# Optimization experiments

Hardware: AMD Instinct MI355X
Metric: run time of the kernel (lower is better)

## Reference

```python
import jax, jax.numpy as jnp
import numpy as np

N_HEADS = 4
NEG_SLOPE = 0.2  # DGL GATConv default leaky_relu slope


def setup_inputs() -> dict:
    key = jax.random.key(0)
    ks = jax.random.split(key, 12)
    N, E = 50000, 800000
    in_dim, time_dim, out_dim = 128, 128, 128
    d_head = out_dim // N_HEADS
    in_total = in_dim + time_dim
    h = jax.random.normal(ks[0], (N, in_dim), jnp.float32)
    time_tensor = jax.random.uniform(ks[1], (E,), jnp.float32)
    src = jax.random.randint(ks[2], (E,), 0, N, jnp.int32)
    dst = jax.random.randint(ks[3], (E,), 0, N, jnp.int32)
    # TimeEncoding: Linear(1, time_dim) with xavier weight, zero bias
    w_t = jax.random.normal(ks[4], (time_dim, 1), jnp.float32) * (6.0 / (1 + time_dim)) ** 0.5
    b_t = jnp.zeros((time_dim,), jnp.float32)
    # GATConv params
    W_fc = jax.random.normal(ks[5], (N_HEADS * d_head, in_total), jnp.float32) * (2.0 / in_total) ** 0.5
    attn_l = jax.random.normal(ks[6], (N_HEADS, d_head), jnp.float32) * 0.1
    attn_r = jax.random.normal(ks[7], (N_HEADS, d_head), jnp.float32) * 0.1
    W_res = jax.random.normal(ks[8], (N_HEADS * d_head, in_total), jnp.float32) * (2.0 / in_total) ** 0.5
    bias = jnp.zeros((N_HEADS * d_head,), jnp.float32)
    return {"h": h, "time_tensor": time_tensor, "src": src, "dst": dst,
            "num_nodes": N, "w_t": w_t, "b_t": b_t, "W_fc": W_fc,
            "attn_l": attn_l, "attn_r": attn_r, "W_res": W_res, "bias": bias}


def reference(h, time_tensor, src, dst, num_nodes, w_t, b_t, W_fc, attn_l, attn_r, W_res, bias):
    N = num_nodes
    E = src.shape[0]
    # Time encoding: cos(W t + b), per edge -> [E, time_dim]
    time_emb = jnp.cos(time_tensor[:, None] * w_t[:, 0][None, :] + b_t[None, :])
    # Mailbox mean of concat([src h, time_emb]) per dst node.
    # mean(concat) == concat(mean, mean), so sum the two halves separately.
    ones = jnp.ones((E,), h.dtype)
    deg = jax.ops.segment_sum(ones, dst, num_segments=N)  # [N]
    sum_h = jax.ops.segment_sum(h[src], dst, num_segments=N)       # [N, in_dim]
    sum_t = jax.ops.segment_sum(time_emb, dst, num_segments=N)     # [N, time_dim]
    inv_deg = 1.0 / jnp.maximum(deg, 1.0)
    h_time = jnp.concatenate([sum_h, sum_t], axis=1) * inv_deg[:, None]  # [N, in+time]
    # GATConv (eval mode, no dropout)
    d_head = W_fc.shape[0] // N_HEADS
    feat = (h_time @ W_fc.T).reshape(N, N_HEADS, d_head)  # [N,H,D]
    el = jnp.sum(feat * attn_l[None], axis=-1)  # [N,H]
    er = jnp.sum(feat * attn_r[None], axis=-1)  # [N,H]
    e = el[src] + er[dst]                        # [E,H]
    e = jnp.where(e > 0, e, NEG_SLOPE * e)
    # edge softmax over incoming edges of each dst node
    m = jax.ops.segment_max(e, dst, num_segments=N)  # [N,H]
    m = jnp.where(jnp.isfinite(m), m, 0.0)
    ex = jnp.exp(e - m[dst])
    denom = jax.ops.segment_sum(ex, dst, num_segments=N)
    a = ex / jnp.maximum(denom[dst], 1e-9)           # [E,H]
    rst = jax.ops.segment_sum(a[:, :, None] * feat[src], dst, num_segments=N)  # [N,H,D]
    res = (h_time @ W_res.T).reshape(N, N_HEADS, d_head)
    out = rst + res + bias.reshape(1, N_HEADS, d_head)
    out = jax.nn.elu(out)
    return out.reshape(N, -1)  # [N, out_dim]
```

## Files before the change

kernel.cpp:

```cpp
#include <hip/hip_runtime.h>
#include <math.h>

#define NH 4
#define NEG_SLOPE 0.2f
#define BKT_SHIFT 8
#define EPB 4096
#define CBLK 8192
#define INV2PI 0.15915494309189535f
#define LOG2E  1.4426950408889634f

typedef __attribute__((ext_vector_type(8))) short bf16x8;
typedef __attribute__((ext_vector_type(4))) float f32x4;

__device__ __forceinline__ float blo(unsigned u) { return __uint_as_float(u << 16); }
__device__ __forceinline__ float bhi(unsigned u) { return __uint_as_float(u & 0xFFFF0000u); }
__device__ __forceinline__ unsigned short rne(float f) {
    unsigned u = __float_as_uint(f);
    u += 0x7FFFu + ((u >> 16) & 1u);
    return (unsigned short)(u >> 16);
}
__device__ __forceinline__ unsigned pack2(float a, float b) {
    return (unsigned)rne(a) | ((unsigned)rne(b) << 16);
}

__global__ __launch_bounds__(256) void k_prep(
    const float* __restrict__ h, unsigned* __restrict__ hbu, int n_pairs,
    const float* __restrict__ Wfc, const float* __restrict__ Wres,
    unsigned* __restrict__ wcat,
    const float* __restrict__ w_t, const float* __restrict__ b_t,
    float2* __restrict__ w_s, float2* __restrict__ b_s,
    const int* __restrict__ dst, int* __restrict__ bkt_cnt, int E, int NB, int EB) {
    __shared__ int cnt[256];
    int tid = threadIdx.x;
    int t = blockIdx.x * blockDim.x + tid;
    if (t < n_pairs) {
        float2 v = ((const float2*)h)[t];
        hbu[t] = pack2(v.x, v.y);
    }
    if (t < 32768) {
        int col = t >> 7, kk = t & 127;
        const float* srcp = (col < 128) ? (Wfc + (size_t)col * 256)
                                        : (Wres + (size_t)(col - 128) * 256);
        float2 v = ((const float2*)srcp)[kk];
        wcat[t] = pack2(v.x, v.y);
    }
    if (t < 64) {
        float2 wv = ((const float2*)w_t)[t];
        float2 bv = ((const float2*)b_t)[t];
        w_s[t] = make_float2(wv.x * INV2PI, wv.y * INV2PI);
        b_s[t] = make_float2(bv.x * INV2PI, bv.y * INV2PI);
    }
    if (blockIdx.x < (unsigned)EB) {
        cnt[tid] = 0;
        __syncthreads();
        int q0 = (blockIdx.x * CBLK) >> 2;
#pragma unroll
        for (int k = 0; k < CBLK / 1024; k++) {
            int qi = q0 + k * 256 + tid;
            int base = qi * 4;
            if (base + 3 < E) {
                int4 d = ((const int4*)dst)[qi];
                atomicAdd(&cnt[d.x >> BKT_SHIFT], 1);
                atomicAdd(&cnt[d.y >> BKT_SHIFT], 1);
                atomicAdd(&cnt[d.z >> BKT_SHIFT], 1);
                atomicAdd(&cnt[d.w >> BKT_SHIFT], 1);
            } else {
                for (int e = base; e < E; e++) atomicAdd(&cnt[dst[e] >> BKT_SHIFT], 1);
            }
        }
        __syncthreads();
        if (tid < NB) {
            int c = cnt[tid];
            if (c) atomicAdd(bkt_cnt + tid, c);
        }
    }
}

__global__ __launch_bounds__(256) void k_bktscan(
    const int* __restrict__ bkt_cnt, int* __restrict__ bkt_start,
    int* __restrict__ bkt_cursor, int* __restrict__ row_start,
    int NB, int E, int N) {
    __shared__ int wsum[4];
    int tid = threadIdx.x, lane = tid & 63, wid = tid >> 6;
    int v = (tid < NB) ? bkt_cnt[tid] : 0;
    int x = v;
#pragma unroll
    for (int off = 1; off < 64; off <<= 1) {
        int y = __shfl_up(x, off, 64);
        if (lane >= off) x += y;
    }
    if (lane == 63) wsum[wid] = x;
    __syncthreads();
    if (tid == 0) {
        int s = 0;
#pragma unroll
        for (int k = 0; k < 4; k++) { int tk = wsum[k]; wsum[k] = s; s += tk; }
    }
    __syncthreads();
    int excl = wsum[wid] + x - v;
    if (tid < NB) { bkt_start[tid] = excl; bkt_cursor[tid] = excl; }
    if (tid == 0) { bkt_start[NB] = E; row_start[N] = E; }
}

__global__ __launch_bounds__(256) void k_binscatter(
    const int* __restrict__ src, const int* __restrict__ dst,
    const float* __restrict__ tt, int* __restrict__ bkt_cursor,
    uint2* __restrict__ staged, int E, int NB) {
    __shared__ int cnt[1024];
    __shared__ int basep[1024];
    int e0 = blockIdx.x * EPB;
    int tid = threadIdx.x;
    for (int b = tid; b < NB; b += 256) cnt[b] = 0;
    __syncthreads();
#pragma unroll
    for (int k = 0; k < EPB / 256; k++) {
        int e = e0 + k * 256 + tid;
        if (e < E) atomicAdd(&cnt[dst[e] >> BKT_SHIFT], 1);
    }
    __syncthreads();
    for (int b = tid; b < NB; b += 256) {
        int c = cnt[b];
        basep[b] = (c > 0) ? atomicAdd(bkt_cursor + b, c) : 0;
        cnt[b] = 0;
    }
    __syncthreads();
#pragma unroll
    for (int k = 0; k < EPB / 256; k++) {
        int e = e0 + k * 256 + tid;
        if (e < E) {
            int d = dst[e];
            int b = d >> BKT_SHIFT;
            int r = atomicAdd(&cnt[b], 1);
            unsigned tq = min((unsigned)(tt[e] * 32768.0f), 32767u);
            staged[basep[b] + r] =
                make_uint2(((unsigned)src[e] << 15) | tq, (unsigned)(d & 255));
        }
    }
}

__global__ __launch_bounds__(256) void k_binsort(
    const uint2* __restrict__ staged, const int* __restrict__ bkt_start,
    int* __restrict__ row_start, unsigned* __restrict__ est, int N) {
    __shared__ int cnt[256];
    __shared__ int cur[256];
    __shared__ int wsum[4];
    int b = blockIdx.x;
    int n0 = b << BKT_SHIFT;
    int tid = threadIdx.x;
    cnt[tid] = 0;
    __syncthreads();
    int s0 = bkt_start[b], s1 = bkt_start[b + 1];
    for (int p = s0 + tid; p < s1; p += 256)
        atomicAdd(&cnt[staged[p].y], 1);
    __syncthreads();
    int lane = tid & 63, wid = tid >> 6;
    int v = cnt[tid];
    int x = v;
#pragma unroll
    for (int off = 1; off < 64; off <<= 1) {
        int y = __shfl_up(x, off, 64);
        if (lane >= off) x += y;
    }
    if (lane == 63) wsum[wid] = x;
    __syncthreads();
    if (tid == 0) {
        int s = 0;
#pragma unroll
        for (int k = 0; k < 4; k++) { int tk = wsum[k]; wsum[k] = s; s += tk; }
    }
    __syncthreads();
    int excl = s0 + wsum[wid] + x - v;
    cur[tid] = excl;
    if (n0 + tid < N) row_start[n0 + tid] = excl;
    __syncthreads();
    for (int p = s0 + tid; p < s1; p += 256) {
        uint2 vv = staged[p];
        int pos = atomicAdd(&cur[vv.y], 1);
        est[pos] = vv.x;
    }
}

__device__ __forceinline__ void agg_edge(unsigned u, const uint4* __restrict__ h4,
                                         int i, float4 wa, float4 wb, float4 ba, float4 bb,
                                         float* aH, float* aT) {
    int s = (int)(u >> 15);
    float t = (float)((u & 0x7FFFu)) * (1.0f / 32768.0f) + (0.5f / 32768.0f);
    uint4 hv = h4[(size_t)s * 16 + i];
    aH[0] += blo(hv.x); aH[1] += bhi(hv.x);
    aH[2] += blo(hv.y); aH[3] += bhi(hv.y);
    aH[4] += blo(hv.z); aH[5] += bhi(hv.z);
    aH[6] += blo(hv.w); aH[7] += bhi(hv.w);
    aT[0] += __builtin_amdgcn_cosf(fmaf(t, wa.x, ba.x));
    aT[1] += __builtin_amdgcn_cosf(fmaf(t, wa.y, ba.y));
    aT[2] += __builtin_amdgcn_cosf(fmaf(t, wa.z, ba.z));
    aT[3] += __builtin_amdgcn_cosf(fmaf(t, wa.w, ba.w));
    aT[4] += __builtin_amdgcn_cosf(fmaf(t, wb.x, bb.x));
    aT[5] += __builtin_amdgcn_cosf(fmaf(t, wb.y, bb.y));
    aT[6] += __builtin_amdgcn_cosf(fmaf(t, wb.z, bb.z));
    aT[7] += __builtin_amdgcn_cosf(fmaf(t, wb.w, bb.w));
}

__device__ __forceinline__ void attn_edge(unsigned u, const uint4* __restrict__ f4,
                                          int i, int hd, const float* __restrict__ el,
                                          float erh, float* acc, float& den) {
    int s = (int)(u >> 15);
    float elh = el[(size_t)s * 4 + hd];
    uint4 fv = f4[(size_t)s * 16 + i];
    float w = elh + erh; w = w > 0.f ? w : NEG_SLOPE * w;
    float ex = __builtin_amdgcn_exp2f(w);
    acc[0] = fmaf(ex, blo(fv.x), acc[0]); acc[1] = fmaf(ex, bhi(fv.x), acc[1]);
    acc[2] = fmaf(ex, blo(fv.y), acc[2]); acc[3] = fmaf(ex, bhi(fv.y), acc[3]);
    acc[4] = fmaf(ex, blo(fv.z), acc[4]); acc[5] = fmaf(ex, bhi(fv.z), acc[5]);
    acc[6] = fmaf(ex, blo(fv.w), acc[6]); acc[7] = fmaf(ex, bhi(fv.w), acc[7]);
    den += ex;
}

__global__ __launch_bounds__(256) void k_agg(
    const unsigned* __restrict__ hbu, const unsigned* __restrict__ est,
    const int* __restrict__ row_start,
    const float2* __restrict__ w_s, const float2* __restrict__ b_s,
    unsigned* __restrict__ htu, int N) {
    int n = blockIdx.x * 4 + (threadIdx.x >> 6);
    if (n >= N) return;
    int lane = threadIdx.x & 63;
    int g = lane >> 4, i = lane & 15;
    int rs = row_start[n], re = row_start[n + 1];
    const uint4* h4 = (const uint4*)hbu;
    float4 wa = ((const float4*)w_s)[2 * i], wb = ((const float4*)w_s)[2 * i + 1];
    float4 ba = ((const float4*)b_s)[2 * i], bb = ((const float4*)b_s)[2 * i + 1];
    float aH[8] = {}, aT[8] = {};
    int nb = (re - rs) >> 4;
    int e = rs + g;
    for (int j = 0; j < nb; j++, e += 16) {
        unsigned u0 = est[e];
        unsigned u1 = est[e + 4];
        unsigned u2 = est[e + 8];
        unsigned u3 = est[e + 12];
        agg_edge(u0, h4, i, wa, wb, ba, bb, aH, aT);
        agg_edge(u1, h4, i, wa, wb, ba, bb, aH, aT);
        agg_edge(u2, h4, i, wa, wb, ba, bb, aH, aT);
        agg_edge(u3, h4, i, wa, wb, ba, bb, aH, aT);
    }
    for (; e < re; e += 4)
        agg_edge(est[e], h4, i, wa, wb, ba, bb, aH, aT);
#pragma unroll
    for (int off = 16; off <= 32; off <<= 1) {
#pragma unroll
        for (int k = 0; k < 8; k++) {
            aH[k] += __shfl_xor(aH[k], off, 64);
            aT[k] += __shfl_xor(aT[k], off, 64);
        }
    }
    if (g == 0) {
        int deg = re - rs;
        float idg = (deg > 0) ? 1.0f / (float)deg : 1.0f;
        uint4* ht4 = (uint4*)htu;
        uint4 oh, ot;
        oh.x = pack2(aH[0] * idg, aH[1] * idg);
        oh.y = pack2(aH[2] * idg, aH[3] * idg);
        oh.z = pack2(aH[4] * idg, aH[5] * idg);
        oh.w = pack2(aH[6] * idg, aH[7] * idg);
        ot.x = pack2(aT[0] * idg, aT[1] * idg);
        ot.y = pack2(aT[2] * idg, aT[3] * idg);
        ot.z = pack2(aT[4] * idg, aT[5] * idg);
        ot.w = pack2(aT[6] * idg, aT[7] * idg);
        ht4[(size_t)n * 32 + i]      = oh;
        ht4[(size_t)n * 32 + 16 + i] = ot;
    }
}

__global__ __launch_bounds__(256) void k_gemm(
    const unsigned short* __restrict__ ht, const unsigned short* __restrict__ wcat,
    unsigned short* __restrict__ feat, float* __restrict__ res_out,
    const float* __restrict__ attn_l, const float* __restrict__ attn_r,
    float* __restrict__ el, float* __restrict__ er, int N) {
    __shared__ __align__(16) unsigned short As[64 * 264];
    int tid = threadIdx.x;
    int row0 = blockIdx.x * 64;
    const uint4* src4 = (const uint4*)ht;
    for (int idx = tid; idx < 64 * 32; idx += 256) {
        int rl = idx >> 5, c16 = idx & 31;
        int gr = row0 + rl; if (gr >= N) gr = N - 1;
        uint4 v = src4[(size_t)gr * 32 + c16];
        *(uint4*)(As + rl * 264 + c16 * 8) = v;
    }
    __syncthreads();
    int wave = tid >> 6, lane = tid & 63;
    int r = lane & 15, q = lane >> 4;
    int colbase = wave * 64;
    const bf16x8* bbase = (const bf16x8*)wcat + (size_t)(colbase + r) * 32;
    const unsigned short* abase = As + r * 264 + q * 8;
    f32x4 acc[4][4] = {};
#pragma unroll
    for (int ks = 0; ks < 8; ks++) {
        bf16x8 a[4], b[4];
#pragma unroll
        for (int rt = 0; rt < 4; rt++)
            a[rt] = *(const bf16x8*)(abase + rt * (16 * 264) + ks * 32);
#pragma unroll
        for (int ct = 0; ct < 4; ct++)
            b[ct] = bbase[(size_t)ct * (16 * 32) + ks * 4 + q];
#pragma unroll
        for (int rt = 0; rt < 4; rt++)
#pragma unroll
            for (int ct = 0; ct < 4; ct++)
                acc[rt][ct] = __builtin_amdgcn_mfma_f32_16x16x32_bf16(a[rt], b[ct], acc[rt][ct], 0, 0, 0);
    }
    bool featw = (colbase < 128);
    float alv[4], arv[4];
    if (featw) {
#pragma unroll
        for (int ct = 0; ct < 4; ct++) {
            alv[ct] = attn_l[colbase + ct * 16 + r];
            arv[ct] = attn_r[colbase + ct * 16 + r];
        }
    }
#pragma unroll
    for (int rt = 0; rt < 4; rt++) {
#pragma unroll
        for (int reg = 0; reg < 4; reg++) {
            int row = row0 + rt * 16 + q * 4 + reg;
            float el0 = 0.f, el1 = 0.f, er0 = 0.f, er1 = 0.f;
#pragma unroll
            for (int ct = 0; ct < 4; ct++) {
                int col = colbase + ct * 16 + r;
                float v = acc[rt][ct][reg];
                if (featw) {
                    unsigned short pv = rne(v);
                    if (row < N) feat[(size_t)row * 128 + col] = pv;
                    float vr = blo((unsigned)pv);
                    if (ct < 2) { el0 = fmaf(vr, alv[ct], el0); er0 = fmaf(vr, arv[ct], er0); }
                    else        { el1 = fmaf(vr, alv[ct], el1); er1 = fmaf(vr, arv[ct], er1); }
                } else {
                    if (row < N) res_out[(size_t)row * 128 + (col - 128)] = v;
                }
            }
            if (featw) {
#pragma unroll
                for (int off = 1; off <= 8; off <<= 1) {
                    el0 += __shfl_xor(el0, off, 64);
                    el1 += __shfl_xor(el1, off, 64);
                    er0 += __shfl_xor(er0, off, 64);
                    er1 += __shfl_xor(er1, off, 64);
                }
                if (r == 0 && row < N) {
                    int hd0 = colbase >> 5;
                    el[(size_t)row * 4 + hd0]     = el0 * LOG2E;
                    el[(size_t)row * 4 + hd0 + 1] = el1 * LOG2E;
                    er[(size_t)row * 4 + hd0]     = er0 * LOG2E;
                    er[(size_t)row * 4 + hd0 + 1] = er1 * LOG2E;
                }
            }
        }
    }
}

__global__ __launch_bounds__(256) void k_attn(
    const unsigned* __restrict__ est, const int* __restrict__ row_start,
    const float* __restrict__ el, const float* __restrict__ er,
    const unsigned* __restrict__ featu, const float* __restrict__ bias,
    float* __restrict__ out, int N) {
    int n = blockIdx.x * 4 + (threadIdx.x >> 6);
    if (n >= N) return;
    int lane = threadIdx.x & 63;
    int g = lane >> 4, i = lane & 15;
    int hd = i >> 2;
    int rs = row_start[n], re = row_start[n + 1];
    float erh = er[(size_t)n * 4 + hd];
    const uint4* f4 = (const uint4*)featu;
    float acc[8] = {};
    float den = 0.f;
    int nb = (re - rs) >> 4;
    int e = rs + g;
    for (int j = 0; j < nb; j++, e += 16) {
        unsigned u0 = est[e];
        unsigned u1 = est[e + 4];
        unsigned u2 = est[e + 8];
        unsigned u3 = est[e + 12];
        attn_edge(u0, f4, i, hd, el, erh, acc, den);
        attn_edge(u1, f4, i, hd, el, erh, acc, den);
        attn_edge(u2, f4, i, hd, el, erh, acc, den);
        attn_edge(u3, f4, i, hd, el, erh, acc, den);
    }
    for (; e < re; e += 4)
        attn_edge(est[e], f4, i, hd, el, erh, acc, den);
#pragma unroll
    for (int off = 16; off <= 32; off <<= 1) {
#pragma unroll
        for (int k = 0; k < 8; k++) acc[k] += __shfl_xor(acc[k], off, 64);
        den += __shfl_xor(den, off, 64);
    }
    if (g == 0) {
        float id = 1.0f / fmaxf(den, 1e-9f);
        float* op = out + (size_t)n * 128 + i * 8;
        const float* bp = bias + i * 8;
        float4 o0 = ((const float4*)op)[0], o1 = ((const float4*)op)[1];
        float4 b0 = ((const float4*)bp)[0], b1 = ((const float4*)bp)[1];
        float4 r0, r1;
        r0.x = fmaf(acc[0], id, o0.x + b0.x);
        r0.y = fmaf(acc[1], id, o0.y + b0.y);
        r0.z = fmaf(acc[2], id, o0.z + b0.z);
        r0.w = fmaf(acc[3], id, o0.w + b0.w);
        r1.x = fmaf(acc[4], id, o1.x + b1.x);
        r1.y = fmaf(acc[5], id, o1.y + b1.y);
        r1.z = fmaf(acc[6], id, o1.z + b1.z);
        r1.w = fmaf(acc[7], id, o1.w + b1.w);
        r0.x = r0.x > 0.f ? r0.x : (__expf(r0.x) - 1.0f);
        r0.y = r0.y > 0.f ? r0.y : (__expf(r0.y) - 1.0f);
        r0.z = r0.z > 0.f ? r0.z : (__expf(r0.z) - 1.0f);
        r0.w = r0.w > 0.f ? r0.w : (__expf(r0.w) - 1.0f);
        r1.x = r1.x > 0.f ? r1.x : (__expf(r1.x) - 1.0f);
        r1.y = r1.y > 0.f ? r1.y : (__expf(r1.y) - 1.0f);
        r1.z = r1.z > 0.f ? r1.z : (__expf(r1.z) - 1.0f);
        r1.w = r1.w > 0.f ? r1.w : (__expf(r1.w) - 1.0f);
        ((float4*)op)[0] = r0;
        ((float4*)op)[1] = r1;
    }
}

extern "C" void kernel_launch(void* const* d_in, const int* in_sizes, int n_in,
                              void* d_out, int out_size, void* d_ws, size_t ws_size,
                              hipStream_t stream) {
    const float* h     = (const float*)d_in[0];
    const float* tt    = (const float*)d_in[1];
    const int*   src   = (const int*)d_in[2];
    const int*   dst   = (const int*)d_in[3];
    const float* w_t   = (const float*)d_in[5];
    const float* b_t   = (const float*)d_in[6];
    const float* W_fc  = (const float*)d_in[7];
    const float* al    = (const float*)d_in[8];
    const float* ar    = (const float*)d_in[9];
    const float* W_res = (const float*)d_in[10];
    const float* bias  = (const float*)d_in[11];

    int N = in_sizes[0] / 128;
    int E = in_sizes[1];
    int NB = (N + 255) >> BKT_SHIFT;
    int EB = (E + CBLK - 1) / CBLK;

    char* ws = (char*)d_ws;
    size_t off = 0;
    auto alloc = [&](size_t bytes) { void* p = ws + off; off = (off + bytes + 15) & ~(size_t)15; return p; };
    unsigned* htu     = (unsigned*)alloc((size_t)N * 128 * 4);
    unsigned* hbu     = (unsigned*)alloc((size_t)N * 64 * 4);
    unsigned* featu   = (unsigned*)alloc((size_t)N * 64 * 4);
    unsigned* wcat    = (unsigned*)alloc(32768 * 4);
    float2*   w_s     = (float2*)alloc(64 * 8);
    float2*   b_s     = (float2*)alloc(64 * 8);
    float*    el      = (float*)alloc((size_t)N * NH * 4);
    float*    er      = (float*)alloc((size_t)N * NH * 4);
    int*      row_st  = (int*)alloc((size_t)(N + 1) * 4);
    int*      bkt_cur = (int*)alloc((size_t)NB * 4);
    int*      bkt_cnt = (int*)alloc((size_t)NB * 4);
    int*      bkt_sta = (int*)alloc((size_t)(NB + 1) * 4);
    unsigned* est     = (unsigned*)alloc((size_t)E * 4);
    uint2*    staged  = (uint2*)featu;

    hipMemsetAsync(bkt_cnt, 0, (size_t)NB * 4, stream);

    int prep_n = N * 64;
    hipLaunchKernelGGL(k_prep, dim3((prep_n + 255) / 256), dim3(256), 0, stream,
                       h, hbu, prep_n, W_fc, W_res, wcat, w_t, b_t, w_s, b_s,
                       dst, bkt_cnt, E, NB, EB);
    hipLaunchKernelGGL(k_bktscan, dim3(1), dim3(256), 0, stream,
                       bkt_cnt, bkt_sta, bkt_cur, row_st, NB, E, N);
    hipLaunchKernelGGL(k_binscatter, dim3((E + EPB - 1) / EPB), dim3(256), 0, stream,
                       src, dst, tt, bkt_cur, staged, E, NB);
    hipLaunchKernelGGL(k_binsort, dim3(NB), dim3(256), 0, stream,
                       staged, bkt_sta, row_st, est, N);
    hipLaunchKernelGGL(k_agg, dim3((N + 3) / 4), dim3(256), 0, stream,
                       hbu, est, row_st, w_s, b_s, htu, N);
    hipLaunchKernelGGL(k_gemm, dim3((N + 63) / 64), dim3(256), 0, stream,
                       (const unsigned short*)htu, (const unsigned short*)wcat,
                       (unsigned short*)featu, (float*)d_out, al, ar, el, er, N);
    hipLaunchKernelGGL(k_attn, dim3((N + 3) / 4), dim3(256), 0, stream,
                       est, row_st, el, er, featu, bias, (float*)d_out, N);
}
```

Baseline: 252.1 us.

## Shrink GEMM tile to 16 rows without LDS and split el/er into separate kernel

The GEMM kernel drops its 64-row LDS-staged A tile and instead has each wave load its 16-row A fragment straight from global memory, launching four times as many blocks. The el/er attention-logit reduction moves out of the GEMM epilogue into a new small kernel that re-reads the bf16 feat rows. This removes the LDS stage, the shuffle reductions and register pressure from the GEMM, which may raise occupancy. In exchange it cuts reuse of each B-tile load across rows, repeats A loads across the four waves, and adds a kernel launch plus an extra pass over feat.

```diff
diff --git a/kernel.cpp b/kernel.cpp
--- a/kernel.cpp
+++ b/kernel.cpp
@@ -271,88 +271,62 @@
 
 __global__ __launch_bounds__(256) void k_gemm(
     const unsigned short* __restrict__ ht, const unsigned short* __restrict__ wcat,
-    unsigned short* __restrict__ feat, float* __restrict__ res_out,
-    const float* __restrict__ attn_l, const float* __restrict__ attn_r,
-    float* __restrict__ el, float* __restrict__ er, int N) {
-    __shared__ __align__(16) unsigned short As[64 * 264];
+    unsigned short* __restrict__ feat, float* __restrict__ res_out, int N) {
     int tid = threadIdx.x;
-    int row0 = blockIdx.x * 64;
-    const uint4* src4 = (const uint4*)ht;
-    for (int idx = tid; idx < 64 * 32; idx += 256) {
-        int rl = idx >> 5, c16 = idx & 31;
-        int gr = row0 + rl; if (gr >= N) gr = N - 1;
-        uint4 v = src4[(size_t)gr * 32 + c16];
-        *(uint4*)(As + rl * 264 + c16 * 8) = v;
-    }
-    __syncthreads();
     int wave = tid >> 6, lane = tid & 63;
     int r = lane & 15, q = lane >> 4;
+    int row0 = blockIdx.x * 16;
     int colbase = wave * 64;
+    int gr = row0 + r; if (gr >= N) gr = N - 1;
+    const bf16x8* a_base = (const bf16x8*)ht + (size_t)gr * 32;
     const bf16x8* bbase = (const bf16x8*)wcat + (size_t)(colbase + r) * 32;
-    const unsigned short* abase = As + r * 264 + q * 8;
-    f32x4 acc[4][4] = {};
+    f32x4 acc[4] = {};
 #pragma unroll
     for (int ks = 0; ks < 8; ks++) {
-        bf16x8 a[4], b[4];
-#pragma unroll
-        for (int rt = 0; rt < 4; rt++)
-            a[rt] = *(const bf16x8*)(abase + rt * (16 * 264) + ks * 32);
+        bf16x8 a = a_base[ks * 4 + q];
+        bf16x8 b[4];
 #pragma unroll
         for (int ct = 0; ct < 4; ct++)
             b[ct] = bbase[(size_t)ct * (16 * 32) + ks * 4 + q];
 #pragma unroll
-        for (int rt = 0; rt < 4; rt++)
-#pragma unroll
-            for (int ct = 0; ct < 4; ct++)
-                acc[rt][ct] = __builtin_amdgcn_mfma_f32_16x16x32_bf16(a[rt], b[ct], acc[rt][ct], 0, 0, 0);
+        for (int ct = 0; ct < 4; ct++)
+            acc[ct] = __builtin_amdgcn_mfma_f32_16x16x32_bf16(a, b[ct], acc[ct], 0, 0, 0);
     }
     bool featw = (colbase < 128);
-    float alv[4], arv[4];
-    if (featw) {
-#pragma unroll
-        for (int ct = 0; ct < 4; ct++) {
-            alv[ct] = attn_l[colbase + ct * 16 + r];
-            arv[ct] = attn_r[colbase + ct * 16 + r];
+#pragma unroll
+    for (int ct = 0; ct < 4; ct++) {
+        int col = colbase + ct * 16 + r;
+#pragma unroll
+        for (int reg = 0; reg < 4; reg++) {
+            int row = row0 + q * 4 + reg;
+            if (row >= N) continue;
+            float v = acc[ct][reg];
+            if (featw) feat[(size_t)row * 128 + col] = rne(v);
+            else       res_out[(size_t)row * 128 + (col - 128)] = v;
         }
     }
-#pragma unroll
-    for (int rt = 0; rt < 4; rt++) {
-#pragma unroll
-        for (int reg = 0; reg < 4; reg++) {
-            int row = row0 + rt * 16 + q * 4 + reg;
-            float el0 = 0.f, el1 = 0.f, er0 = 0.f, er1 = 0.f;
-#pragma unroll
-            for (int ct = 0; ct < 4; ct++) {
-                int col = colbase + ct * 16 + r;
-                float v = acc[rt][ct][reg];
-                if (featw) {
-                    unsigned short pv = rne(v);
-                    if (row < N) feat[(size_t)row * 128 + col] = pv;
-                    float vr = blo((unsigned)pv);
-                    if (ct < 2) { el0 = fmaf(vr, alv[ct], el0); er0 = fmaf(vr, arv[ct], er0); }
-                    else        { el1 = fmaf(vr, alv[ct], el1); er1 = fmaf(vr, arv[ct], er1); }
-                } else {
-                    if (row < N) res_out[(size_t)row * 128 + (col - 128)] = v;
-                }
-            }
-            if (featw) {
-#pragma unroll
-                for (int off = 1; off <= 8; off <<= 1) {
-                    el0 += __shfl_xor(el0, off, 64);
-                    el1 += __shfl_xor(el1, off, 64);
-                    er0 += __shfl_xor(er0, off, 64);
-                    er1 += __shfl_xor(er1, off, 64);
-                }
-                if (r == 0 && row < N) {
-                    int hd0 = colbase >> 5;
-                    el[(size_t)row * 4 + hd0]     = el0 * LOG2E;
-                    el[(size_t)row * 4 + hd0 + 1] = el1 * LOG2E;
-                    er[(size_t)row * 4 + hd0]     = er0 * LOG2E;
-                    er[(size_t)row * 4 + hd0 + 1] = er1 * LOG2E;
-                }
-            }
-        }
-    }
+}
+
+__global__ void k_el_er(const unsigned* __restrict__ featu,
+                        const float* __restrict__ attn_l, const float* __restrict__ attn_r,
+                        float* __restrict__ el, float* __restrict__ er, int NH4) {
+    int t = blockIdx.x * blockDim.x + threadIdx.x;
+    if (t >= NH4) return;
+    int n = t >> 2, hd = t & 3;
+    const unsigned* f = featu + (size_t)n * 64 + hd * 16;
+    const float2* al = (const float2*)(attn_l + hd * 32);
+    const float2* ar = (const float2*)(attn_r + hd * 32);
+    float sl = 0.f, sr = 0.f;
+#pragma unroll
+    for (int i = 0; i < 16; i++) {
+        unsigned u = f[i];
+        float f0 = blo(u), f1 = bhi(u);
+        float2 a = al[i], b = ar[i];
+        sl = fmaf(f0, a.x, fmaf(f1, a.y, sl));
+        sr = fmaf(f0, b.x, fmaf(f1, b.y, sr));
+    }
+    el[t] = sl * LOG2E;
+    er[t] = sr * LOG2E;
 }
 
 __global__ __launch_bounds__(256) void k_attn(
@@ -470,9 +444,11 @@
                        staged, bkt_sta, row_st, est, N);
     hipLaunchKernelGGL(k_agg, dim3((N + 3) / 4), dim3(256), 0, stream,
                        hbu, est, row_st, w_s, b_s, htu, N);
-    hipLaunchKernelGGL(k_gemm, dim3((N + 63) / 64), dim3(256), 0, stream,
+    hipLaunchKernelGGL(k_gemm, dim3((N + 15) / 16), dim3(256), 0, stream,
                        (const unsigned short*)htu, (const unsigned short*)wcat,
-                       (unsigned short*)featu, (float*)d_out, al, ar, el, er, N);
+                       (unsigned short*)featu, (float*)d_out, N);
+    hipLaunchKernelGGL(k_el_er, dim3((N * NH + 255) / 256), dim3(256), 0, stream,
+                       featu, al, ar, el, er, N * NH);
     hipLaunchKernelGGL(k_attn, dim3((N + 3) / 4), dim3(256), 0, stream,
                        est, row_st, el, er, featu, bias, (float*)d_out, N);
 }
```

Result: slower. 281.3 us (+11.6%).
